# Kernel tuning notes

Measured on AMD Instinct MI355X. Metric: run time of the kernel, lower is better.

Reference implementation:

```python
import jax, jax.numpy as jnp
import numpy as np

N = 50000      # num nodes
E = 800000     # num edges
F_IN = 100     # input features (ogbn-products)
HID = 128      # hidden_dim (per-head out_channels)
H = 2          # heads
OUT = 47       # num classes
NEG_SLOPE = 0.2


def setup_inputs() -> dict:
    key = jax.random.key(0)
    ks = jax.random.split(key, 14)
    def glorot(k, shape, fan):
        return jax.random.normal(k, shape, jnp.float32) * (1.0 / np.sqrt(fan))
    x = jax.random.normal(ks[0], (N, F_IN), jnp.float32)
    edge_index = jax.random.randint(ks[1], (2, E), 0, N)
    # GAT layer 0: lin_l (= lin_r, shared) weight [H*HID, F_IN], attention vecs [H, HID]
    W0 = glorot(ks[2], (H * HID, F_IN), F_IN)
    b0 = jnp.zeros((H * HID,), jnp.float32)
    attl0 = glorot(ks[3], (H, HID), HID)
    attr0 = glorot(ks[4], (H, HID), HID)
    # GAT layer 1: input dim H*HID
    W1 = glorot(ks[5], (H * HID, H * HID), H * HID)
    b1 = jnp.zeros((H * HID,), jnp.float32)
    attl1 = glorot(ks[6], (H, HID), HID)
    attr1 = glorot(ks[7], (H, HID), HID)
    # post_mp: Linear(H*HID -> HID), Linear(HID -> OUT)
    Wp1 = glorot(ks[8], (HID, H * HID), H * HID)
    bp1 = jnp.zeros((HID,), jnp.float32)
    Wp2 = glorot(ks[9], (OUT, HID), HID)
    bp2 = jnp.zeros((OUT,), jnp.float32)
    return dict(x=x, edge_index=edge_index, W0=W0, b0=b0, attl0=attl0, attr0=attr0,
                W1=W1, b1=b1, attl1=attl1, attr1=attr1,
                Wp1=Wp1, bp1=bp1, Wp2=Wp2, bp2=bp2)


def gat_layer(x, W, b, att_l, att_r, src, dst):
    # shared lin_l == lin_r in the source
    h = (x @ W.T + b).reshape(-1, H, HID)          # [N, H, C]
    alpha_l = jnp.einsum('nhc,hc->nh', h, att_l)   # per-node left scores
    alpha_r = jnp.einsum('nhc,hc->nh', h, att_r)   # per-node right scores
    e = jax.nn.leaky_relu(alpha_l[src] + alpha_r[dst], NEG_SLOPE)  # [E, H]
    # segment softmax over edges grouped by destination node
    emax = jax.ops.segment_max(e, dst, num_segments=N)             # [N, H]
    ee = jnp.exp(e - emax[dst])
    denom = jax.ops.segment_sum(ee, dst, num_segments=N)           # [N, H]
    a = ee / denom[dst]                                            # [E, H]
    msg = a[:, :, None] * h[src]                                   # [E, H, C]
    out = jax.ops.segment_sum(msg, dst, num_segments=N)            # [N, H, C]
    return out.reshape(-1, H * HID)


def reference(x, edge_index, W0, b0, attl0, attr0, W1, b1, attl1, attr1, Wp1, bp1, Wp2, bp2):
    src, dst = edge_index[0], edge_index[1]
    x = jax.nn.relu(gat_layer(x, W0, b0, attl0, attr0, src, dst))
    x = jax.nn.relu(gat_layer(x, W1, b1, attl1, attr1, src, dst))
    h = x @ Wp1.T + bp1           # dropout p=0.0 -> identity
    logits = h @ Wp2.T + bp2
    return jax.nn.log_softmax(logits, axis=1)
```

## Files before the change

kernel.cpp:

```cpp
#include <hip/hip_runtime.h>
#include <math.h>

#define N_NODES 50000
#define E_EDGES 800000
#define F_IN 100
#define HID 128
#define HEADS 2
#define OUT_C 47
#define HH (HEADS*HID)
#define MPAD 50176
#define SLOTS 64
#define NGEMM (MPAD/32)
#define NEB 3136

typedef float floatx4 __attribute__((ext_vector_type(4)));
typedef float float2v __attribute__((ext_vector_type(2)));
typedef short short8 __attribute__((ext_vector_type(8)));

__device__ inline ushort bf16round(float v) {
    unsigned u = __float_as_uint(v);
    return (ushort)((u + 0x7FFFu + ((u >> 16) & 1u)) >> 16);
}

__device__ __forceinline__ void gl_lds16(const void* g, void* l) {
    __builtin_amdgcn_global_load_lds(
        (const __attribute__((address_space(1))) unsigned int*)g,
        (__attribute__((address_space(3))) unsigned int*)l, 16, 0, 0);
}

__device__ __forceinline__ void epi2h(
    const floatx4* acc,
    const float* __restrict__ bias,
    const float* __restrict__ attl, const float* __restrict__ attr,
    ushort* __restrict__ Hb, float* __restrict__ al, float* __restrict__ ar,
    int m0, int wave, int lane)
{
    const int quad = lane >> 4, l16 = lane & 15;
#pragma unroll
    for (int h = 0; h < 2; h++) {
        float bias_r[8], att_l[8], att_r[8];
#pragma unroll
        for (int sn = 0; sn < 8; sn++) {
            int ai = h * 128 + sn * 16 + l16;
            bias_r[sn] = bias[ai];
            att_l[sn] = attl[ai];
            att_r[sn] = attr[ai];
        }
#pragma unroll
        for (int r = 0; r < 4; r++) {
            int gm = m0 + wave * 16 + quad * 4 + r;
            float suml = 0.f, sumr = 0.f;
#pragma unroll
            for (int sn = 0; sn < 8; sn++) {
                float v = acc[h * 8 + sn][r] + bias_r[sn];
                suml += v * att_l[sn];
                sumr += v * att_r[sn];
                if (gm < N_NODES) {
                    int gn = h * 128 + sn * 16 + l16;
                    Hb[(size_t)gm * 256 + gn] = bf16round(v);
                }
            }
#pragma unroll
            for (int off = 1; off < 16; off <<= 1) {
                suml += __shfl_xor(suml, off);
                sumr += __shfl_xor(sumr, off);
            }
            if (l16 == 0 && gm < N_NODES) {
                al[gm * HEADS + h] = suml;
                ar[gm * HEADS + h] = sumr;
            }
        }
    }
}

__global__ void prep(int* __restrict__ deg,
                     const float* __restrict__ W0, const float* __restrict__ W1,
                     const float* __restrict__ Wp1, const float* __restrict__ Wp2,
                     ushort* __restrict__ W0b, ushort* __restrict__ W1b,
                     ushort* __restrict__ Wp1b, ushort* __restrict__ Wp2b) {
    const int c0 = 256 * 32;
    const int c1 = c0 + (HH * HH) / 4;
    const int c2 = c1 + (HID * HH) / 4;
    const int c3 = c2 + (64 * HID) / 4;
    int i = blockIdx.x * 256 + threadIdx.x;
    if (i < N_NODES) deg[i] = 0;
    if (i >= c3) return;
    float4 v = make_float4(0.f, 0.f, 0.f, 0.f);
    ushort* H; size_t o;
    if (i < c0) {
        int row = i >> 5, kc = (i & 31) * 4;
        if (kc < F_IN) v = *(const float4*)(W0 + (size_t)row * F_IN + kc);
        H = W0b; o = (size_t)row * 128 + kc;
    } else if (i < c1) {
        int j = i - c0;
        v = *(const float4*)(W1 + (size_t)j * 4);
        H = W1b; o = (size_t)j * 4;
    } else if (i < c2) {
        int j = i - c1;
        v = *(const float4*)(Wp1 + (size_t)j * 4);
        H = Wp1b; o = (size_t)j * 4;
    } else {
        int j = i - c2;
        int row = j >> 5;
        if (row < OUT_C) v = *(const float4*)(Wp2 + (size_t)j * 4);
        H = Wp2b; o = (size_t)j * 4;
    }
    ushort4 r;
    r.x = bf16round(v.x); r.y = bf16round(v.y);
    r.z = bf16round(v.z); r.w = bf16round(v.w);
    *(ushort4*)(H + o) = r;
}

__global__ __launch_bounds__(128) void gemm_l0_edges(
    const float* __restrict__ x, const ushort* __restrict__ W0b,
    const float* __restrict__ b0,
    const float* __restrict__ attl0, const float* __restrict__ attr0,
    ushort* __restrict__ hb, float* __restrict__ al, float* __restrict__ ar,
    const int* __restrict__ srcv, const int* __restrict__ dstv,
    int* __restrict__ deg, ushort* __restrict__ csr16)
{
    __shared__ ushort sA[32 * 32];
    __shared__ ushort sB[256 * 32];
    const int g = blockIdx.x;
    if (g % 3 == 0) {
        const int by = g / 3;
        const int t = threadIdx.x;
        const int wave = t >> 6, lane = t & 63;
        const int quad = lane >> 4, l16 = lane & 15;
        const int rl = lane >> 2, seg = lane & 3;
        const int m0 = by * 32;

        floatx4 acc[16];
#pragma unroll
        for (int j = 0; j < 16; j++) acc[j] = (floatx4)(0.f);

        for (int k0 = 0; k0 < 128; k0 += 32) {
#pragma unroll
            for (int rnd = 0; rnd < 2; rnd++) {
                int row = wave * 16 + (lane >> 3) + rnd * 8;
                int c4 = (lane & 7) * 4;
                int col = k0 + c4;
                int gmr = m0 + row;
                float4 v = make_float4(0.f, 0.f, 0.f, 0.f);
                if (gmr < N_NODES && col < F_IN)
                    v = *(const float4*)(x + (size_t)gmr * F_IN + col);
                ushort4 u;
                u.x = bf16round(v.x); u.y = bf16round(v.y);
                u.z = bf16round(v.z); u.w = bf16round(v.w);
                *(ushort4*)(sA + row * 32 + c4) = u;
            }
#pragma unroll
            for (int j = 0; j < 8; j++) {
                int br = wave * 128 + j * 16;
                size_t gro = (size_t)(br + rl) * 128 + k0 + seg * 8;
                gl_lds16(W0b + gro, sB + br * 32);
            }
            __syncthreads();
            short8 af = *(const short8*)(sA + (wave * 16 + l16) * 32 + quad * 8);
#pragma unroll
            for (int sn = 0; sn < 16; sn++) {
                short8 b = *(const short8*)(sB + (sn * 16 + l16) * 32 + quad * 8);
                acc[sn] = __builtin_amdgcn_mfma_f32_16x16x32_bf16(af, b, acc[sn], 0, 0, 0);
            }
            __syncthreads();
        }
        epi2h(acc, b0, attl0, attr0, hb, al, ar, m0, wave, lane);
    } else {
        const int eidx = g - g / 3 - 1;
        int e0 = eidx * 256 + threadIdx.x;
#pragma unroll
        for (int rep = 0; rep < 2; rep++) {
            int e = e0 + rep * 128;
            if (e < E_EDGES) {
                int d = dstv[e];
                int r = atomicAdd(&deg[d], 1);
                if (r < SLOTS) csr16[(size_t)d * SLOTS + r] = (ushort)srcv[e];
            }
        }
    }
}

__global__ __launch_bounds__(128) void gemm_l1(
    const ushort* __restrict__ Ab, const ushort* __restrict__ Wb,
    const float* __restrict__ bias, ushort* __restrict__ Hb,
    const float* __restrict__ attl, const float* __restrict__ attr,
    float* __restrict__ al, float* __restrict__ ar)
{
    __shared__ ushort sA[32 * 32];
    __shared__ ushort sB[256 * 32];
    const int t = threadIdx.x;
    const int wave = t >> 6, lane = t & 63;
    const int quad = lane >> 4, l16 = lane & 15;
    const int rl = lane >> 2, seg = lane & 3;
    const int m0 = blockIdx.x * 32;

    floatx4 acc[16];
#pragma unroll
    for (int j = 0; j < 16; j++) acc[j] = (floatx4)(0.f);

    for (int k0 = 0; k0 < HH; k0 += 32) {
        {
            size_t gro = (size_t)(m0 + wave * 16 + rl) * HH + k0 + seg * 8;
            gl_lds16(Ab + gro, sA + (wave * 16) * 32);
        }
#pragma unroll
        for (int j = 0; j < 8; j++) {
            int br = wave * 128 + j * 16;
            size_t gro = (size_t)(br + rl) * HH + k0 + seg * 8;
            gl_lds16(Wb + gro, sB + br * 32);
        }
        __syncthreads();
        short8 af = *(const short8*)(sA + (wave * 16 + l16) * 32 + quad * 8);
#pragma unroll
        for (int sn = 0; sn < 16; sn++) {
            short8 b = *(const short8*)(sB + (sn * 16 + l16) * 32 + quad * 8);
            acc[sn] = __builtin_amdgcn_mfma_f32_16x16x32_bf16(af, b, acc[sn], 0, 0, 0);
        }
        __syncthreads();
    }
    epi2h(acc, bias, attl, attr, Hb, al, ar, m0, wave, lane);
}

__global__ __launch_bounds__(256) void gat_aggregate(
    const ushort* __restrict__ hb, const float* __restrict__ al, const float* __restrict__ ar,
    const int* __restrict__ deg, const ushort* __restrict__ csr16,
    ushort* __restrict__ outb)
{
    const int g = blockIdx.x;
    const int xcd = g & 7;
    const int head = xcd & 1;
    const int rank = (g >> 3) * 4 + (xcd >> 1);
    const int wave = threadIdx.x >> 6;
    const int node = rank * 4 + wave;
    const int lane = threadIdx.x & 63;
    const int grp = lane >> 4, c = lane & 15;
    const int n = min(deg[node], SLOTS);
    const float ard = ar[node * HEADS + head];
    const ushort* __restrict__ hbh = hb + head * HID + c * 8;

    float dsum = 0.f;
    float2v av[4];
#pragma unroll
    for (int j = 0; j < 4; j++) av[j] = (float2v)(0.f);

    int s = 0; float w = 0.f;
    if (lane < n) {
        s = (int)csr16[(size_t)node * SLOTS + lane];
        float e = al[s * HEADS + head] + ard;
        e = fmaxf(e, 0.f) + 0.2f * fminf(e, 0.f);
        w = __expf(e);
        dsum = w;
    }
    const int nn = (n + 7) & ~7;
    for (int i = 0; i < nn; i += 8) {
        int e0 = i + grp, e1 = i + 4 + grp;
        int   s0 = __shfl(s, e0);
        float w0 = __shfl(w, e0);
        int   s1 = __shfl(s, e1);
        float w1 = __shfl(w, e1);
        uint4 q0 = *(const uint4*)(hbh + (size_t)s0 * 256);
        uint4 q1 = *(const uint4*)(hbh + (size_t)s1 * 256);
        float2v we0 = (float2v)(w0);
        float2v we1 = (float2v)(w1);
        float2v p;
        p.x = __uint_as_float(q0.x << 16); p.y = __uint_as_float(q0.x & 0xFFFF0000u);
        av[0] += we0 * p;
        p.x = __uint_as_float(q0.y << 16); p.y = __uint_as_float(q0.y & 0xFFFF0000u);
        av[1] += we0 * p;
        p.x = __uint_as_float(q0.z << 16); p.y = __uint_as_float(q0.z & 0xFFFF0000u);
        av[2] += we0 * p;
        p.x = __uint_as_float(q0.w << 16); p.y = __uint_as_float(q0.w & 0xFFFF0000u);
        av[3] += we0 * p;
        p.x = __uint_as_float(q1.x << 16); p.y = __uint_as_float(q1.x & 0xFFFF0000u);
        av[0] += we1 * p;
        p.x = __uint_as_float(q1.y << 16); p.y = __uint_as_float(q1.y & 0xFFFF0000u);
        av[1] += we1 * p;
        p.x = __uint_as_float(q1.z << 16); p.y = __uint_as_float(q1.z & 0xFFFF0000u);
        av[2] += we1 * p;
        p.x = __uint_as_float(q1.w << 16); p.y = __uint_as_float(q1.w & 0xFFFF0000u);
        av[3] += we1 * p;
    }
#pragma unroll
    for (int j = 0; j < 4; j++) {
        av[j].x += __shfl_xor(av[j].x, 16);
        av[j].y += __shfl_xor(av[j].y, 16);
        av[j].x += __shfl_xor(av[j].x, 32);
        av[j].y += __shfl_xor(av[j].y, 32);
    }
#pragma unroll
    for (int off = 32; off; off >>= 1) dsum += __shfl_xor(dsum, off);

    if (grp == 0) {
        const float inv = (n > 0) ? 1.f / dsum : 0.f;
        ushort r[8];
#pragma unroll
        for (int j = 0; j < 4; j++) {
            r[2*j]   = bf16round(fmaxf(av[j].x * inv, 0.f));
            r[2*j+1] = bf16round(fmaxf(av[j].y * inv, 0.f));
        }
        *(uint4*)(outb + (size_t)node * 256 + head * HID + c * 8) = *(uint4*)r;
    }
}

__global__ __launch_bounds__(128) void fused_post(
    const ushort* __restrict__ Ab,
    const ushort* __restrict__ Bb,
    const float* __restrict__ bp1,
    const ushort* __restrict__ W2b,
    const float* __restrict__ bp2,
    float* __restrict__ out, int M)
{
    __shared__ ushort sA[32 * 32];
    __shared__ ushort sB[128 * 32];
    __shared__ ushort sP[32 * 136];

    const int t = threadIdx.x;
    const int wave = t >> 6, lane = t & 63;
    const int quad = lane >> 4, l16 = lane & 15;
    const int rl = lane >> 2, seg = lane & 3;
    const int m0 = blockIdx.x * 32;

    floatx4 acc[8];
#pragma unroll
    for (int j = 0; j < 8; j++) acc[j] = (floatx4)(0.f);

    for (int k0 = 0; k0 < HH; k0 += 32) {
        {
            size_t gro = (size_t)(m0 + wave * 16 + rl) * HH + k0 + seg * 8;
            gl_lds16(Ab + gro, sA + (wave * 16) * 32);
        }
#pragma unroll
        for (int j = 0; j < 4; j++) {
            int br = wave * 64 + j * 16;
            size_t gro = (size_t)(br + rl) * HH + k0 + seg * 8;
            gl_lds16(Bb + gro, sB + br * 32);
        }
        __syncthreads();
        short8 af = *(const short8*)(sA + (wave * 16 + l16) * 32 + quad * 8);
#pragma unroll
        for (int sn = 0; sn < 8; sn++) {
            short8 b = *(const short8*)(sB + (sn * 16 + l16) * 32 + quad * 8);
            acc[sn] = __builtin_amdgcn_mfma_f32_16x16x32_bf16(af, b, acc[sn], 0, 0, 0);
        }
        __syncthreads();
    }
#pragma unroll
    for (int sn = 0; sn < 8; sn++)
#pragma unroll
        for (int r = 0; r < 4; r++) {
            int row = wave * 16 + quad * 4 + r;
            int col = sn * 16 + l16;
            sP[row * 136 + col] = bf16round(acc[sn][r] + bp1[col]);
        }
    __syncthreads();

    floatx4 acc2[4];
#pragma unroll
    for (int j = 0; j < 4; j++) acc2[j] = (floatx4)(0.f);

    for (int k0 = 0; k0 < HID; k0 += 32) {
#pragma unroll
        for (int j = 0; j < 2; j++) {
            int br = wave * 32 + j * 16;
            size_t gro = (size_t)(br + rl) * HID + k0 + seg * 8;
            gl_lds16(W2b + gro, sB + br * 32);
        }
        __syncthreads();
        short8 ph = *(const short8*)(sP + (wave * 16 + l16) * 136 + k0 + quad * 8);
#pragma unroll
        for (int sn = 0; sn < 4; sn++) {
            short8 b = *(const short8*)(sB + (sn * 16 + l16) * 32 + quad * 8);
            acc2[sn] = __builtin_amdgcn_mfma_f32_16x16x32_bf16(ph, b, acc2[sn], 0, 0, 0);
        }
        __syncthreads();
    }

    float b2[4];
#pragma unroll
    for (int sn = 0; sn < 4; sn++) {
        int n = sn * 16 + l16;
        b2[sn] = (n < OUT_C) ? bp2[n] : 0.f;
    }
#pragma unroll
    for (int r = 0; r < 4; r++) {
        float v[4];
        float m = -INFINITY;
#pragma unroll
        for (int sn = 0; sn < 4; sn++) {
            int n = sn * 16 + l16;
            float xv = (n < OUT_C) ? acc2[sn][r] + b2[sn] : -INFINITY;
            v[sn] = xv;
            m = fmaxf(m, xv);
        }
#pragma unroll
        for (int off = 1; off < 16; off <<= 1) m = fmaxf(m, __shfl_xor(m, off));
        float ssum = 0.f;
#pragma unroll
        for (int sn = 0; sn < 4; sn++) {
            int n = sn * 16 + l16;
            if (n < OUT_C) ssum += __expf(v[sn] - m);
        }
#pragma unroll
        for (int off = 1; off < 16; off <<= 1) ssum += __shfl_xor(ssum, off);
        float lse = m + logf(ssum);
        int gm = m0 + wave * 16 + quad * 4 + r;
        if (gm < M) {
#pragma unroll
            for (int sn = 0; sn < 4; sn++) {
                int n = sn * 16 + l16;
                if (n < OUT_C) out[(size_t)gm * OUT_C + n] = v[sn] - lse;
            }
        }
    }
}

extern "C" void kernel_launch(void* const* d_in, const int* in_sizes, int n_in,
                              void* d_out, int out_size, void* d_ws, size_t ws_size,
                              hipStream_t stream) {
    const float* x     = (const float*)d_in[0];
    const int*   ei    = (const int*)d_in[1];
    const float* W0    = (const float*)d_in[2];
    const float* b0    = (const float*)d_in[3];
    const float* attl0 = (const float*)d_in[4];
    const float* attr0 = (const float*)d_in[5];
    const float* W1    = (const float*)d_in[6];
    const float* b1    = (const float*)d_in[7];
    const float* attl1 = (const float*)d_in[8];
    const float* attr1 = (const float*)d_in[9];
    const float* Wp1   = (const float*)d_in[10];
    const float* bp1   = (const float*)d_in[11];
    const float* Wp2   = (const float*)d_in[12];
    const float* bp2   = (const float*)d_in[13];
    float* out = (float*)d_out;

    const int Nn = N_NODES, Etot = E_EDGES;
    const int* srcv = ei;
    const int* dstv = ei + Etot;

    char* ws = (char*)d_ws;
    size_t off = 0;
    auto alloc = [&](size_t bytes) -> void* {
        void* p = ws + off;
        off = (off + bytes + 255) & ~(size_t)255;
        return p;
    };
    int*    deg    = (int*)alloc((size_t)Nn * sizeof(int));
    ushort* csr16  = (ushort*)alloc((size_t)Nn * SLOTS * 2);
    float*  al     = (float*)alloc((size_t)Nn * HEADS * sizeof(float));
    float*  ar     = (float*)alloc((size_t)Nn * HEADS * sizeof(float));
    ushort* W0b    = (ushort*)alloc((size_t)HH * 128 * 2);
    ushort* W1b    = (ushort*)alloc((size_t)HH * HH * 2);
    ushort* Wp1b   = (ushort*)alloc((size_t)HID * HH * 2);
    ushort* Wp2b   = (ushort*)alloc((size_t)64 * HID * 2);
    ushort* hb     = (ushort*)alloc((size_t)MPAD * HH * 2);
    ushort* xbb    = (ushort*)alloc((size_t)MPAD * HH * 2);

    prep<<<196, 256, 0, stream>>>(deg, W0, W1, Wp1, Wp2, W0b, W1b, Wp1b, Wp2b);

    gemm_l0_edges<<<NGEMM + NEB, 128, 0, stream>>>(
        x, W0b, b0, attl0, attr0, hb, al, ar, srcv, dstv, deg, csr16);

    gat_aggregate<<<25000, 256, 0, stream>>>(hb, al, ar, deg, csr16, xbb);

    gemm_l1<<<NGEMM, 128, 0, stream>>>(xbb, W1b, b1, hb, attl1, attr1, al, ar);

    gat_aggregate<<<25000, 256, 0, stream>>>(hb, al, ar, deg, csr16, xbb);

    fused_post<<<NGEMM, 128, 0, stream>>>(xbb, Wp1b, bp1, Wp2b, bp2, out, Nn);
}
```

Measured before the change: 285.7 us.

## Make layer-1 and post-MLP GEMMs persistent with whole weight resident in LDS

The layer-1 GEMM and the fused post-MP kernel become persistent kernels: 256 blocks of 512 threads each load the entire bf16 weight matrix once into LDS, with an XOR swizzle applied by the prep kernel to avoid bank conflicts. Each wave then loops over 16-row tiles, reading A fragments straight from global memory into registers, with no per-K-step syncthreads. This removes the repeated weight reloads and barrier overhead of the old 32-row tiles. In exchange it uses 128KB of LDS per block, which limits occupancy to one block per CU, and the A loads from global are uncoalesced.

Result: slower. 451.4 us (+58.0%).

```diff
diff --git a/kernel.cpp b/kernel.cpp
--- a/kernel.cpp
+++ b/kernel.cpp
@@ -10,8 +10,9 @@
 #define HH (HEADS*HID)
 #define MPAD 50176
 #define SLOTS 64
-#define NGEMM (MPAD/32)
+#define NGEMM 1568
 #define NEB 3136
+#define NT16 (MPAD/16)
 
 typedef float floatx4 __attribute__((ext_vector_type(4)));
 typedef float float2v __attribute__((ext_vector_type(2)));
@@ -79,9 +80,9 @@
                      ushort* __restrict__ W0b, ushort* __restrict__ W1b,
                      ushort* __restrict__ Wp1b, ushort* __restrict__ Wp2b) {
     const int c0 = 256 * 32;
-    const int c1 = c0 + (HH * HH) / 4;
-    const int c2 = c1 + (HID * HH) / 4;
-    const int c3 = c2 + (64 * HID) / 4;
+    const int c1 = c0 + 16384;
+    const int c2 = c1 + 8192;
+    const int c3 = c2 + 2048;
     int i = blockIdx.x * 256 + threadIdx.x;
     if (i < N_NODES) deg[i] = 0;
     if (i >= c3) return;
@@ -92,18 +93,17 @@
         if (kc < F_IN) v = *(const float4*)(W0 + (size_t)row * F_IN + kc);
         H = W0b; o = (size_t)row * 128 + kc;
     } else if (i < c1) {
-        int j = i - c0;
+        int j = i - c0; int row = j >> 6, c4 = j & 63;
         v = *(const float4*)(W1 + (size_t)j * 4);
-        H = W1b; o = (size_t)j * 4;
+        H = W1b; o = (size_t)row * 256 + ((c4 ^ ((row & 7) << 1)) << 2);
     } else if (i < c2) {
-        int j = i - c1;
+        int j = i - c1; int row = j >> 6, c4 = j & 63;
         v = *(const float4*)(Wp1 + (size_t)j * 4);
-        H = Wp1b; o = (size_t)j * 4;
+        H = Wp1b; o = (size_t)row * 256 + ((c4 ^ ((row & 7) << 1)) << 2);
     } else {
-        int j = i - c2;
-        int row = j >> 5;
+        int j = i - c2; int row = j >> 5, c4 = j & 31;
         if (row < OUT_C) v = *(const float4*)(Wp2 + (size_t)j * 4);
-        H = Wp2b; o = (size_t)j * 4;
+        H = Wp2b; o = (size_t)row * 128 + ((c4 ^ ((row & 7) << 1)) << 2);
     }
     ushort4 r;
     r.x = bf16round(v.x); r.y = bf16round(v.y);
@@ -180,45 +180,43 @@
     }
 }
 
-__global__ __launch_bounds__(128) void gemm_l1(
-    const ushort* __restrict__ Ab, const ushort* __restrict__ Wb,
+__global__ __launch_bounds__(512) void gemm_l1_persist(
+    const ushort* __restrict__ Ab, const ushort* __restrict__ Wswz,
     const float* __restrict__ bias, ushort* __restrict__ Hb,
     const float* __restrict__ attl, const float* __restrict__ attr,
     float* __restrict__ al, float* __restrict__ ar)
 {
-    __shared__ ushort sA[32 * 32];
-    __shared__ ushort sB[256 * 32];
+    __shared__ ushort sB[256 * 256];
     const int t = threadIdx.x;
     const int wave = t >> 6, lane = t & 63;
     const int quad = lane >> 4, l16 = lane & 15;
-    const int rl = lane >> 2, seg = lane & 3;
-    const int m0 = blockIdx.x * 32;
-
-    floatx4 acc[16];
-#pragma unroll
-    for (int j = 0; j < 16; j++) acc[j] = (floatx4)(0.f);
-
-    for (int k0 = 0; k0 < HH; k0 += 32) {
-        {
-            size_t gro = (size_t)(m0 + wave * 16 + rl) * HH + k0 + seg * 8;
-            gl_lds16(Ab + gro, sA + (wave * 16) * 32);
-        }
-#pragma unroll
-        for (int j = 0; j < 8; j++) {
-            int br = wave * 128 + j * 16;
-            size_t gro = (size_t)(br + rl) * HH + k0 + seg * 8;
-            gl_lds16(Wb + gro, sB + br * 32);
-        }
-        __syncthreads();
-        short8 af = *(const short8*)(sA + (wave * 16 + l16) * 32 + quad * 8);
-#pragma unroll
-        for (int sn = 0; sn < 16; sn++) {
-            short8 b = *(const short8*)(sB + (sn * 16 + l16) * 32 + quad * 8);
-            acc[sn] = __builtin_amdgcn_mfma_f32_16x16x32_bf16(af, b, acc[sn], 0, 0, 0);
-        }
-        __syncthreads();
-    }
-    epi2h(acc, bias, attl, attr, Hb, al, ar, m0, wave, lane);
+#pragma unroll
+    for (int i = 0; i < 16; i++) {
+        int c = i * 512 + wave * 64;
+        gl_lds16(Wswz + (size_t)c * 8 + lane * 8, sB + (size_t)c * 8);
+    }
+    __syncthreads();
+    const int swz = (l16 & 7) << 3;
+    for (int tt = blockIdx.x * 8 + wave; tt < NT16; tt += 2048) {
+        const int m0 = tt * 16;
+        short8 af[8];
+#pragma unroll
+        for (int ks = 0; ks < 8; ks++)
+            af[ks] = *(const short8*)(Ab + (size_t)(m0 + l16) * HH + ks * 32 + quad * 8);
+        floatx4 acc[16];
+#pragma unroll
+        for (int j = 0; j < 16; j++) acc[j] = (floatx4)(0.f);
+#pragma unroll
+        for (int ks = 0; ks < 8; ks++) {
+#pragma unroll
+            for (int sn = 0; sn < 16; sn++) {
+                int idx = (((sn * 16 + l16) * 256) + ks * 32 + quad * 8) ^ swz;
+                short8 b = *(const short8*)(sB + idx);
+                acc[sn] = __builtin_amdgcn_mfma_f32_16x16x32_bf16(af[ks], b, acc[sn], 0, 0, 0);
+            }
+        }
+        epi2h(acc, bias, attl, attr, Hb, al, ar, m0, 0, lane);
+    }
 }
 
 __global__ __launch_bounds__(256) void gat_aggregate(
@@ -302,113 +300,107 @@
     }
 }
 
-__global__ __launch_bounds__(128) void fused_post(
-    const ushort* __restrict__ Ab,
-    const ushort* __restrict__ Bb,
-    const float* __restrict__ bp1,
-    const ushort* __restrict__ W2b,
-    const float* __restrict__ bp2,
-    float* __restrict__ out, int M)
+__global__ __launch_bounds__(512) void fused_post_persist(
+    const ushort* __restrict__ Ab, const ushort* __restrict__ B1swz,
+    const float* __restrict__ bp1, const ushort* __restrict__ W2swz,
+    const float* __restrict__ bp2, float* __restrict__ out, int M)
 {
-    __shared__ ushort sA[32 * 32];
-    __shared__ ushort sB[128 * 32];
-    __shared__ ushort sP[32 * 136];
-
+    __shared__ ushort sB1[128 * 256];
+    __shared__ ushort sB2[64 * 128];
+    __shared__ ushort sP[8][16 * 136];
     const int t = threadIdx.x;
     const int wave = t >> 6, lane = t & 63;
     const int quad = lane >> 4, l16 = lane & 15;
-    const int rl = lane >> 2, seg = lane & 3;
-    const int m0 = blockIdx.x * 32;
-
-    floatx4 acc[8];
-#pragma unroll
-    for (int j = 0; j < 8; j++) acc[j] = (floatx4)(0.f);
-
-    for (int k0 = 0; k0 < HH; k0 += 32) {
-        {
-            size_t gro = (size_t)(m0 + wave * 16 + rl) * HH + k0 + seg * 8;
-            gl_lds16(Ab + gro, sA + (wave * 16) * 32);
-        }
-#pragma unroll
-        for (int j = 0; j < 4; j++) {
-            int br = wave * 64 + j * 16;
-            size_t gro = (size_t)(br + rl) * HH + k0 + seg * 8;
-            gl_lds16(Bb + gro, sB + br * 32);
-        }
-        __syncthreads();
-        short8 af = *(const short8*)(sA + (wave * 16 + l16) * 32 + quad * 8);
-#pragma unroll
-        for (int sn = 0; sn < 8; sn++) {
-            short8 b = *(const short8*)(sB + (sn * 16 + l16) * 32 + quad * 8);
-            acc[sn] = __builtin_amdgcn_mfma_f32_16x16x32_bf16(af, b, acc[sn], 0, 0, 0);
-        }
-        __syncthreads();
-    }
-#pragma unroll
-    for (int sn = 0; sn < 8; sn++)
-#pragma unroll
-        for (int r = 0; r < 4; r++) {
-            int row = wave * 16 + quad * 4 + r;
-            int col = sn * 16 + l16;
-            sP[row * 136 + col] = bf16round(acc[sn][r] + bp1[col]);
-        }
+#pragma unroll
+    for (int i = 0; i < 8; i++) {
+        int c = i * 512 + wave * 64;
+        gl_lds16(B1swz + (size_t)c * 8 + lane * 8, sB1 + (size_t)c * 8);
+    }
+#pragma unroll
+    for (int i = 0; i < 2; i++) {
+        int c = i * 512 + wave * 64;
+        gl_lds16(W2swz + (size_t)c * 8 + lane * 8, sB2 + (size_t)c * 8);
+    }
     __syncthreads();
-
-    floatx4 acc2[4];
-#pragma unroll
-    for (int j = 0; j < 4; j++) acc2[j] = (floatx4)(0.f);
-
-    for (int k0 = 0; k0 < HID; k0 += 32) {
-#pragma unroll
-        for (int j = 0; j < 2; j++) {
-            int br = wave * 32 + j * 16;
-            size_t gro = (size_t)(br + rl) * HID + k0 + seg * 8;
-            gl_lds16(W2b + gro, sB + br * 32);
-        }
-        __syncthreads();
-        short8 ph = *(const short8*)(sP + (wave * 16 + l16) * 136 + k0 + quad * 8);
-#pragma unroll
-        for (int sn = 0; sn < 4; sn++) {
-            short8 b = *(const short8*)(sB + (sn * 16 + l16) * 32 + quad * 8);
-            acc2[sn] = __builtin_amdgcn_mfma_f32_16x16x32_bf16(ph, b, acc2[sn], 0, 0, 0);
-        }
-        __syncthreads();
-    }
-
+    const int swz = (l16 & 7) << 3;
+    ushort* myP = sP[wave];
     float b2[4];
 #pragma unroll
     for (int sn = 0; sn < 4; sn++) {
         int n = sn * 16 + l16;
         b2[sn] = (n < OUT_C) ? bp2[n] : 0.f;
     }
-#pragma unroll
-    for (int r = 0; r < 4; r++) {
-        float v[4];
-        float m = -INFINITY;
-#pragma unroll
-        for (int sn = 0; sn < 4; sn++) {
-            int n = sn * 16 + l16;
-            float xv = (n < OUT_C) ? acc2[sn][r] + b2[sn] : -INFINITY;
-            v[sn] = xv;
-            m = fmaxf(m, xv);
-        }
-#pragma unroll
-        for (int off = 1; off < 16; off <<= 1) m = fmaxf(m, __shfl_xor(m, off));
-        float ssum = 0.f;
-#pragma unroll
-        for (int sn = 0; sn < 4; sn++) {
-            int n = sn * 16 + l16;
-            if (n < OUT_C) ssum += __expf(v[sn] - m);
-        }
-#pragma unroll
-        for (int off = 1; off < 16; off <<= 1) ssum += __shfl_xor(ssum, off);
-        float lse = m + logf(ssum);
-        int gm = m0 + wave * 16 + quad * 4 + r;
-        if (gm < M) {
+    for (int tt = blockIdx.x * 8 + wave; tt < NT16; tt += 2048) {
+        const int m0 = tt * 16;
+        short8 af[8];
+#pragma unroll
+        for (int ks = 0; ks < 8; ks++)
+            af[ks] = *(const short8*)(Ab + (size_t)(m0 + l16) * HH + ks * 32 + quad * 8);
+        floatx4 acc[8];
+#pragma unroll
+        for (int j = 0; j < 8; j++) acc[j] = (floatx4)(0.f);
+#pragma unroll
+        for (int ks = 0; ks < 8; ks++) {
+#pragma unroll
+            for (int sn = 0; sn < 8; sn++) {
+                int idx = (((sn * 16 + l16) * 256) + ks * 32 + quad * 8) ^ swz;
+                short8 b = *(const short8*)(sB1 + idx);
+                acc[sn] = __builtin_amdgcn_mfma_f32_16x16x32_bf16(af[ks], b, acc[sn], 0, 0, 0);
+            }
+        }
+#pragma unroll
+        for (int sn = 0; sn < 8; sn++)
+#pragma unroll
+            for (int r = 0; r < 4; r++) {
+                int row = quad * 4 + r;
+                int col = sn * 16 + l16;
+                myP[row * 136 + col] = bf16round(acc[sn][r] + bp1[col]);
+            }
+        short8 pf[4];
+#pragma unroll
+        for (int ks = 0; ks < 4; ks++)
+            pf[ks] = *(const short8*)(myP + l16 * 136 + ks * 32 + quad * 8);
+        floatx4 acc2[4];
+#pragma unroll
+        for (int j = 0; j < 4; j++) acc2[j] = (floatx4)(0.f);
+#pragma unroll
+        for (int ks = 0; ks < 4; ks++) {
+#pragma unroll
+            for (int sn = 0; sn < 4; sn++) {
+                int idx = (((sn * 16 + l16) * 128) + ks * 32 + quad * 8) ^ swz;
+                short8 b = *(const short8*)(sB2 + idx);
+                acc2[sn] = __builtin_amdgcn_mfma_f32_16x16x32_bf16(pf[ks], b, acc2[sn], 0, 0, 0);
+            }
+        }
+#pragma unroll
+        for (int r = 0; r < 4; r++) {
+            float v[4];
+            float m = -INFINITY;
 #pragma unroll
             for (int sn = 0; sn < 4; sn++) {
                 int n = sn * 16 + l16;
-                if (n < OUT_C) out[(size_t)gm * OUT_C + n] = v[sn] - lse;
+                float xv = (n < OUT_C) ? acc2[sn][r] + b2[sn] : -INFINITY;
+                v[sn] = xv;
+                m = fmaxf(m, xv);
+            }
+#pragma unroll
+            for (int off = 1; off < 16; off <<= 1) m = fmaxf(m, __shfl_xor(m, off));
+            float ssum = 0.f;
+#pragma unroll
+            for (int sn = 0; sn < 4; sn++) {
+                int n = sn * 16 + l16;
+                if (n < OUT_C) ssum += __expf(v[sn] - m);
+            }
+#pragma unroll
+            for (int off = 1; off < 16; off <<= 1) ssum += __shfl_xor(ssum, off);
+            float lse = m + logf(ssum);
+            int gm = m0 + quad * 4 + r;
+            if (gm < M) {
+#pragma unroll
+                for (int sn = 0; sn < 4; sn++) {
+                    int n = sn * 16 + l16;
+                    if (n < OUT_C) out[(size_t)gm * OUT_C + n] = v[sn] - lse;
+                }
             }
         }
     }
@@ -462,9 +454,9 @@
 
     gat_aggregate<<<25000, 256, 0, stream>>>(hb, al, ar, deg, csr16, xbb);
 
-    gemm_l1<<<NGEMM, 128, 0, stream>>>(xbb, W1b, b1, hb, attl1, attr1, al, ar);
+    gemm_l1_persist<<<256, 512, 0, stream>>>(xbb, W1b, b1, hb, attl1, attr1, al, ar);
 
     gat_aggregate<<<25000, 256, 0, stream>>>(hb, al, ar, deg, csr16, xbb);
 
-    fused_post<<<NGEMM, 128, 0, stream>>>(xbb, Wp1b, bp1, Wp2b, bp2, out, Nn);
-}
+    fused_post_persist<<<256, 512, 0, stream>>>(xbb, Wp1b, bp1, Wp2b, bp2, out, Nn);
+}
```

## Fold the two post-MP linear layers into one precomputed combined weight

Applied to the files above, without the earlier changes.

Since no nonlinearity sits between the two post-processing linears, the prep kernel now precomputes Wc = Wp2·Wp1 (47x256, padded to 64 rows) and bc = Wp2·bp1 + bp2. The fused post kernel then runs a single 256->64 GEMM per 64-row tile instead of a 256->128 GEMM followed by a 128->64 GEMM, removing the intermediate LDS round trip and half the MFMA work. Prep gains a small serial dot-product loop per output element, and skipping the intermediate bf16 rounding changes numerics slightly.

Result: no change. 286.2 us (+0.1%).

```diff
diff --git a/kernel.cpp b/kernel.cpp
--- a/kernel.cpp
+++ b/kernel.cpp
@@ -10,7 +10,7 @@
 #define HH (HEADS*HID)
 #define MPAD 50176
 #define SLOTS 64
-#define NGEMM (MPAD/32)
+#define NGEMM 1568
 #define NEB 3136
 
 typedef float floatx4 __attribute__((ext_vector_type(4)));
@@ -76,39 +76,49 @@
 __global__ void prep(int* __restrict__ deg,
                      const float* __restrict__ W0, const float* __restrict__ W1,
                      const float* __restrict__ Wp1, const float* __restrict__ Wp2,
+                     const float* __restrict__ bp1, const float* __restrict__ bp2,
                      ushort* __restrict__ W0b, ushort* __restrict__ W1b,
-                     ushort* __restrict__ Wp1b, ushort* __restrict__ Wp2b) {
+                     ushort* __restrict__ Wcb, float* __restrict__ bcb) {
     const int c0 = 256 * 32;
-    const int c1 = c0 + (HH * HH) / 4;
-    const int c2 = c1 + (HID * HH) / 4;
-    const int c3 = c2 + (64 * HID) / 4;
+    const int c1 = c0 + 16384;
+    const int c2 = c1 + 16384;
+    const int c3 = c2 + 64;
     int i = blockIdx.x * 256 + threadIdx.x;
     if (i < N_NODES) deg[i] = 0;
     if (i >= c3) return;
-    float4 v = make_float4(0.f, 0.f, 0.f, 0.f);
-    ushort* H; size_t o;
     if (i < c0) {
         int row = i >> 5, kc = (i & 31) * 4;
+        float4 v = make_float4(0.f, 0.f, 0.f, 0.f);
         if (kc < F_IN) v = *(const float4*)(W0 + (size_t)row * F_IN + kc);
-        H = W0b; o = (size_t)row * 128 + kc;
+        ushort4 r;
+        r.x = bf16round(v.x); r.y = bf16round(v.y);
+        r.z = bf16round(v.z); r.w = bf16round(v.w);
+        *(ushort4*)(W0b + (size_t)row * 128 + kc) = r;
     } else if (i < c1) {
         int j = i - c0;
-        v = *(const float4*)(W1 + (size_t)j * 4);
-        H = W1b; o = (size_t)j * 4;
+        float4 v = *(const float4*)(W1 + (size_t)j * 4);
+        ushort4 r;
+        r.x = bf16round(v.x); r.y = bf16round(v.y);
+        r.z = bf16round(v.z); r.w = bf16round(v.w);
+        *(ushort4*)(W1b + (size_t)j * 4) = r;
     } else if (i < c2) {
         int j = i - c1;
-        v = *(const float4*)(Wp1 + (size_t)j * 4);
-        H = Wp1b; o = (size_t)j * 4;
+        int o = j >> 8, k = j & 255;
+        float acc = 0.f;
+        if (o < OUT_C) {
+            for (int jj = 0; jj < HID; jj++)
+                acc += Wp2[o * HID + jj] * Wp1[(size_t)jj * HH + k];
+        }
+        Wcb[(size_t)o * HH + k] = bf16round(acc);
     } else {
-        int j = i - c2;
-        int row = j >> 5;
-        if (row < OUT_C) v = *(const float4*)(Wp2 + (size_t)j * 4);
-        H = Wp2b; o = (size_t)j * 4;
-    }
-    ushort4 r;
-    r.x = bf16round(v.x); r.y = bf16round(v.y);
-    r.z = bf16round(v.z); r.w = bf16round(v.w);
-    *(ushort4*)(H + o) = r;
+        int o = i - c2;
+        float acc = 0.f;
+        if (o < OUT_C) {
+            for (int jj = 0; jj < HID; jj++) acc += Wp2[o * HID + jj] * bp1[jj];
+            acc += bp2[o];
+        }
+        bcb[o] = acc;
+    }
 }
 
 __global__ __launch_bounds__(128) void gemm_l0_edges(
@@ -302,84 +312,48 @@
     }
 }
 
-__global__ __launch_bounds__(128) void fused_post(
+__global__ __launch_bounds__(256) void fused_post_c(
     const ushort* __restrict__ Ab,
-    const ushort* __restrict__ Bb,
-    const float* __restrict__ bp1,
-    const ushort* __restrict__ W2b,
-    const float* __restrict__ bp2,
+    const ushort* __restrict__ Wcb,
+    const float* __restrict__ bcb,
     float* __restrict__ out, int M)
 {
-    __shared__ ushort sA[32 * 32];
-    __shared__ ushort sB[128 * 32];
-    __shared__ ushort sP[32 * 136];
-
+    __shared__ ushort sA[64 * 32];
+    __shared__ ushort sB[64 * 32];
     const int t = threadIdx.x;
     const int wave = t >> 6, lane = t & 63;
     const int quad = lane >> 4, l16 = lane & 15;
     const int rl = lane >> 2, seg = lane & 3;
-    const int m0 = blockIdx.x * 32;
-
-    floatx4 acc[8];
-#pragma unroll
-    for (int j = 0; j < 8; j++) acc[j] = (floatx4)(0.f);
+    const int m0 = blockIdx.x * 64;
+
+    floatx4 acc[4];
+#pragma unroll
+    for (int j = 0; j < 4; j++) acc[j] = (floatx4)(0.f);
 
     for (int k0 = 0; k0 < HH; k0 += 32) {
         {
             size_t gro = (size_t)(m0 + wave * 16 + rl) * HH + k0 + seg * 8;
             gl_lds16(Ab + gro, sA + (wave * 16) * 32);
         }
-#pragma unroll
-        for (int j = 0; j < 4; j++) {
-            int br = wave * 64 + j * 16;
-            size_t gro = (size_t)(br + rl) * HH + k0 + seg * 8;
-            gl_lds16(Bb + gro, sB + br * 32);
+        {
+            size_t gro = (size_t)(wave * 16 + rl) * HH + k0 + seg * 8;
+            gl_lds16(Wcb + gro, sB + (wave * 16) * 32);
         }
         __syncthreads();
         short8 af = *(const short8*)(sA + (wave * 16 + l16) * 32 + quad * 8);
 #pragma unroll
-        for (int sn = 0; sn < 8; sn++) {
+        for (int sn = 0; sn < 4; sn++) {
             short8 b = *(const short8*)(sB + (sn * 16 + l16) * 32 + quad * 8);
             acc[sn] = __builtin_amdgcn_mfma_f32_16x16x32_bf16(af, b, acc[sn], 0, 0, 0);
         }
         __syncthreads();
     }
-#pragma unroll
-    for (int sn = 0; sn < 8; sn++)
-#pragma unroll
-        for (int r = 0; r < 4; r++) {
-            int row = wave * 16 + quad * 4 + r;
-            int col = sn * 16 + l16;
-            sP[row * 136 + col] = bf16round(acc[sn][r] + bp1[col]);
-        }
-    __syncthreads();
-
-    floatx4 acc2[4];
-#pragma unroll
-    for (int j = 0; j < 4; j++) acc2[j] = (floatx4)(0.f);
-
-    for (int k0 = 0; k0 < HID; k0 += 32) {
-#pragma unroll
-        for (int j = 0; j < 2; j++) {
-            int br = wave * 32 + j * 16;
-            size_t gro = (size_t)(br + rl) * HID + k0 + seg * 8;
-            gl_lds16(W2b + gro, sB + br * 32);
-        }
-        __syncthreads();
-        short8 ph = *(const short8*)(sP + (wave * 16 + l16) * 136 + k0 + quad * 8);
-#pragma unroll
-        for (int sn = 0; sn < 4; sn++) {
-            short8 b = *(const short8*)(sB + (sn * 16 + l16) * 32 + quad * 8);
-            acc2[sn] = __builtin_amdgcn_mfma_f32_16x16x32_bf16(ph, b, acc2[sn], 0, 0, 0);
-        }
-        __syncthreads();
-    }
 
     float b2[4];
 #pragma unroll
     for (int sn = 0; sn < 4; sn++) {
         int n = sn * 16 + l16;
-        b2[sn] = (n < OUT_C) ? bp2[n] : 0.f;
+        b2[sn] = (n < OUT_C) ? bcb[n] : 0.f;
     }
 #pragma unroll
     for (int r = 0; r < 4; r++) {
@@ -388,7 +362,7 @@
 #pragma unroll
         for (int sn = 0; sn < 4; sn++) {
             int n = sn * 16 + l16;
-            float xv = (n < OUT_C) ? acc2[sn][r] + b2[sn] : -INFINITY;
+            float xv = (n < OUT_C) ? acc[sn][r] + b2[sn] : -INFINITY;
             v[sn] = xv;
             m = fmaxf(m, xv);
         }
@@ -450,12 +424,13 @@
     float*  ar     = (float*)alloc((size_t)Nn * HEADS * sizeof(float));
     ushort* W0b    = (ushort*)alloc((size_t)HH * 128 * 2);
     ushort* W1b    = (ushort*)alloc((size_t)HH * HH * 2);
-    ushort* Wp1b   = (ushort*)alloc((size_t)HID * HH * 2);
-    ushort* Wp2b   = (ushort*)alloc((size_t)64 * HID * 2);
+    ushort* Wcb    = (ushort*)alloc((size_t)64 * HH * 2);
+    float*  bcb    = (float*)alloc(64 * sizeof(float));
     ushort* hb     = (ushort*)alloc((size_t)MPAD * HH * 2);
     ushort* xbb    = (ushort*)alloc((size_t)MPAD * HH * 2);
 
-    prep<<<196, 256, 0, stream>>>(deg, W0, W1, Wp1, Wp2, W0b, W1b, Wp1b, Wp2b);
+    prep<<<196, 256, 0, stream>>>(deg, W0, W1, Wp1, Wp2, bp1, bp2,
+                                  W0b, W1b, Wcb, bcb);
 
     gemm_l0_edges<<<NGEMM + NEB, 128, 0, stream>>>(
         x, W0b, b0, attl0, attr0, hb, al, ar, srcv, dstv, deg, csr16);
@@ -466,5 +441,5 @@
 
     gat_aggregate<<<25000, 256, 0, stream>>>(hb, al, ar, deg, csr16, xbb);
 
-    fused_post<<<NGEMM, 128, 0, stream>>>(xbb, Wp1b, bp1, Wp2b, bp2, out, Nn);
-}
+    fused_post_c<<<MPAD / 64, 256, 0, stream>>>(xbb, Wcb, bcb, out, Nn);
+}
```
